# Kernel tuning notes

Hardware: AMD Instinct MI355X
Metric: run time of the kernel (lower is better)

The kernel has to match this reference:

```python
import jax, jax.numpy as jnp
import numpy as np

B, S, IN, H, OUT = 512, 1024, 32, 128, 1


def setup_inputs() -> dict:
    key = jax.random.key(0)
    ks = jax.random.split(key, 7)
    sc = 1.0 / np.sqrt(H)  # torch LSTM/Linear default init scale
    return {
        "x": jax.random.normal(ks[0], (B, S, IN), dtype=jnp.float32),
        "W_ih": jax.random.normal(ks[1], (4 * H, IN), dtype=jnp.float32) * sc,
        "W_hh": jax.random.normal(ks[2], (4 * H, H), dtype=jnp.float32) * sc,
        "b_ih": jax.random.normal(ks[3], (4 * H,), dtype=jnp.float32) * sc,
        "b_hh": jax.random.normal(ks[4], (4 * H,), dtype=jnp.float32) * sc,
        "W_lin": jax.random.normal(ks[5], (OUT, H * S), dtype=jnp.float32) * (1.0 / np.sqrt(H * S)),
        "b_lin": jax.random.normal(ks[6], (OUT,), dtype=jnp.float32) * (1.0 / np.sqrt(H * S)),
    }


def _lstm(x, W_ih, W_hh, b_ih, b_hh):
    # x: [B,S,IN]. Precompute input projection for all timesteps (one big GEMM).
    xw = jnp.einsum("bsi,gi->bsg", x, W_ih) + (b_ih + b_hh)  # [B,S,4H]
    h0 = jnp.zeros((x.shape[0], W_hh.shape[1]), dtype=x.dtype)
    c0 = jnp.zeros_like(h0)

    def step(carry, xw_t):
        h, c = carry
        gates = xw_t + h @ W_hh.T  # [B,4H]
        i, f, g, o = jnp.split(gates, 4, axis=-1)  # torch gate order i,f,g,o
        i = jax.nn.sigmoid(i)
        f = jax.nn.sigmoid(f)
        g = jnp.tanh(g)
        o = jax.nn.sigmoid(o)
        c = f * c + i * g
        h = o * jnp.tanh(c)
        return (h, c), h

    (_, _), hs = jax.lax.scan(step, (h0, c0), jnp.swapaxes(xw, 0, 1))  # hs: [S,B,H]
    return jnp.swapaxes(hs, 0, 1)  # [B,S,H]


def reference(x, W_ih, W_hh, b_ih, b_hh, W_lin, b_lin):
    lstm_out = _lstm(x, W_ih, W_hh, b_ih, b_hh)          # [B,S,H]
    flat = lstm_out.reshape(lstm_out.shape[0], -1)        # [B,S*H]
    return flat @ W_lin.T + b_lin                         # [B,OUT]
```

## Files before the change

### kernel.cpp

```cpp
#include <hip/hip_runtime.h>
#include <stdint.h>

constexpr int B = 512, S = 1024, IN = 32, H = 128;
constexpr int KTOT = IN + H;
constexpr int NJ = 4;
constexpr int KSL = KTOT / NJ;
constexpr int KP = KSL / 2;

typedef uint32_t u32;

__device__ __forceinline__ void dot2(float& c, u32 a, u32 b) {
  asm("v_dot2_f32_f16 %0, %1, %2, %0" : "+v"(c) : "v"(a), "v"(b));
}
__device__ __forceinline__ float sigm(float v) {
  float e = __builtin_amdgcn_exp2f(-1.4426950408889634f * v);
  return __builtin_amdgcn_rcpf(1.0f + e);
}
__device__ __forceinline__ float tanh_(float v) {
  float e = __builtin_amdgcn_exp2f(-2.8853900817779268f * v);
  return 2.0f * __builtin_amdgcn_rcpf(1.0f + e) - 1.0f;
}

__global__ __launch_bounds__(512, 4)
void lstm_fused(const float* __restrict__ x, const float* __restrict__ Wih,
                const float* __restrict__ Whh, const float* __restrict__ bih,
                const float* __restrict__ bhh, const float* __restrict__ Wlin,
                const float* __restrict__ blin, float* __restrict__ out) {
  __shared__ alignas(16) _Float16 hx[2][KTOT];
  __shared__ alignas(16) float red[NJ][H][4];
  __shared__ float redf[H];

  const int tid = threadIdx.x;
  const int lane = tid & 63;
  const int w = tid >> 6;
  const int j = w >> 1;
  const int g = (w & 1) * 64 + lane;
  const int b = blockIdx.x;
  const int par = b & 1;
  const int aw0 = par, aw1 = 6 + par;
  const bool isact = (w == aw0) || (w == aw1);
  const int ga = (w == aw0) ? lane : 64 + lane;
  const int xw = 2 + par;

  u32 wreg[4][KP];
#pragma unroll
  for (int c = 0; c < 4; ++c) {
    const int n = c * H + g;
#pragma unroll
    for (int pq = 0; pq < KP; ++pq) {
      const int k0 = KSL * j + 2 * pq, k1 = k0 + 1;
      const float f0 = (k0 < IN) ? Wih[n * IN + k0] : Whh[n * H + (k0 - IN)];
      const float f1 = (k1 < IN) ? Wih[n * IN + k1] : Whh[n * H + (k1 - IN)];
      union { _Float16 h[2]; u32 u; } cv;
      cv.h[0] = (_Float16)f0;
      cv.h[1] = (_Float16)f1;
      wreg[c][pq] = cv.u;
    }
  }
#pragma unroll
  for (int c = 0; c < 4; ++c)
#pragma unroll
    for (int pq = 0; pq < KP; ++pq) asm volatile("" : "+v"(wreg[c][pq]));

  float bias_a[4] = {0.f, 0.f, 0.f, 0.f};
  if (isact) {
#pragma unroll
    for (int c = 0; c < 4; ++c) bias_a[c] = bih[c * H + ga] + bhh[c * H + ga];
  }

  const size_t xbase = (size_t)b * S * IN;
  if (tid < KTOT) {
    hx[0][tid] = (tid < IN) ? (_Float16)x[xbase + tid] : (_Float16)0.0f;
    hx[1][tid] = (_Float16)0.0f;
  }
  __syncthreads();

  float cc = 0.f, oa = 0.f;

  for (int s = 0; s < S; ++s) {
    const int p = s & 1, np = p ^ 1;
    float wl = 0.f, xn = 0.f;
    if (isact) wl = Wlin[s * H + ga];
    const bool xload = (w == xw) && (lane < IN) && (s + 1 < S);
    if (xload) xn = x[xbase + (s + 1) * IN + lane];

    const uint4* pp =
        (const uint4*)((const char*)&hx[p][0] + j * (KSL * 2));
    float acc[4] = {0.f, 0.f, 0.f, 0.f};
#pragma unroll
    for (int q = 0; q < 5; ++q) {
      const uint4 v = pp[q];
      const u32 e[4] = {v.x, v.y, v.z, v.w};
#pragma unroll
      for (int u = 0; u < 4; ++u)
#pragma unroll
        for (int c = 0; c < 4; ++c) dot2(acc[c], e[u], wreg[c][4 * q + u]);
    }
    *(float4*)&red[j][g][0] = make_float4(acc[0], acc[1], acc[2], acc[3]);
    __syncthreads();

    if (isact) {
      const float4 r0 = *(const float4*)&red[0][ga][0];
      const float4 r1 = *(const float4*)&red[1][ga][0];
      const float4 r2 = *(const float4*)&red[2][ga][0];
      const float4 r3 = *(const float4*)&red[3][ga][0];
      const float gi = sigm(r0.x + r1.x + r2.x + r3.x + bias_a[0]);
      const float gf = sigm(r0.y + r1.y + r2.y + r3.y + bias_a[1]);
      const float gg = tanh_(r0.z + r1.z + r2.z + r3.z + bias_a[2]);
      const float go = sigm(r0.w + r1.w + r2.w + r3.w + bias_a[3]);
      cc = gf * cc + gi * gg;
      const float h = go * tanh_(cc);
      hx[np][IN + ga] = (_Float16)h;
      oa += h * wl;
    } else if (xload) {
      hx[np][lane] = (_Float16)xn;
    }
    __syncthreads();
  }

  if (isact) redf[ga] = oa;
  __syncthreads();
  if (tid == 0) {
    float sum = blin[0];
    for (int k = 0; k < H; ++k) sum += redf[k];
    out[b] = sum;
  }
}

extern "C" void kernel_launch(void* const* d_in, const int* in_sizes, int n_in,
                              void* d_out, int out_size, void* d_ws, size_t ws_size,
                              hipStream_t stream) {
  const float* x    = (const float*)d_in[0];
  const float* Wih  = (const float*)d_in[1];
  const float* Whh  = (const float*)d_in[2];
  const float* bih  = (const float*)d_in[3];
  const float* bhh  = (const float*)d_in[4];
  const float* Wlin = (const float*)d_in[5];
  const float* blin = (const float*)d_in[6];
  float* outp = (float*)d_out;
  hipLaunchKernelGGL(lstm_fused, dim3(B), dim3(512), 0, stream,
                     x, Wih, Whh, bih, bhh, Wlin, blin, outp);
}
```

Before: 1.264 ms.

## Process two batch rows per block with software-pipelined dot and activation phases

Each block now handles two sequences with 1024 threads. Each wave holds weights for only two gates, and the work is staggered so the activations of one row overlap the dot products of the other row inside each synchronisation interval. The aim is to hide the serial activation latency and the barrier stalls of the recurrence. In exchange, launch bounds drop to one block per CU, there are half as many blocks, and each wave does twice the dot work per step.

```diff
diff --git a/kernel.cpp b/kernel.cpp
--- a/kernel.cpp
+++ b/kernel.cpp
@@ -21,31 +21,34 @@
   return 2.0f * __builtin_amdgcn_rcpf(1.0f + e) - 1.0f;
 }
 
-__global__ __launch_bounds__(512, 4)
+__global__ __launch_bounds__(1024, 1)
 void lstm_fused(const float* __restrict__ x, const float* __restrict__ Wih,
                 const float* __restrict__ Whh, const float* __restrict__ bih,
                 const float* __restrict__ bhh, const float* __restrict__ Wlin,
                 const float* __restrict__ blin, float* __restrict__ out) {
-  __shared__ alignas(16) _Float16 hx[2][KTOT];
-  __shared__ alignas(16) float red[NJ][H][4];
-  __shared__ float redf[H];
+  __shared__ alignas(16) _Float16 hx0[2][KTOT];
+  __shared__ alignas(16) _Float16 hx1[2][KTOT];
+  __shared__ float red0[NJ][4][H];
+  __shared__ float red1[NJ][4][H];
+  __shared__ float redf[2][H];
 
   const int tid = threadIdx.x;
   const int lane = tid & 63;
   const int w = tid >> 6;
-  const int j = w >> 1;
+  const int j = w >> 2;
+  const int cp = (w >> 1) & 1;
   const int g = (w & 1) * 64 + lane;
-  const int b = blockIdx.x;
-  const int par = b & 1;
-  const int aw0 = par, aw1 = 6 + par;
-  const bool isact = (w == aw0) || (w == aw1);
-  const int ga = (w == aw0) ? lane : 64 + lane;
-  const int xw = 2 + par;
+  const int r0 = blockIdx.x * 2;
 
-  u32 wreg[4][KP];
+  const bool isact0 = (w == 0) || (w == 5);
+  const bool isact1 = (w == 10) || (w == 15);
+  const bool isact = isact0 || isact1;
+  const int ga = ((w == 5) || (w == 15)) ? 64 + lane : lane;
+
+  u32 wreg[2][KP];
 #pragma unroll
-  for (int c = 0; c < 4; ++c) {
-    const int n = c * H + g;
+  for (int c2 = 0; c2 < 2; ++c2) {
+    const int n = (2 * cp + c2) * H + g;
 #pragma unroll
     for (int pq = 0; pq < KP; ++pq) {
       const int k0 = KSL * j + 2 * pq, k1 = k0 + 1;
@@ -54,77 +57,103 @@
       union { _Float16 h[2]; u32 u; } cv;
       cv.h[0] = (_Float16)f0;
       cv.h[1] = (_Float16)f1;
-      wreg[c][pq] = cv.u;
+      wreg[c2][pq] = cv.u;
     }
   }
 #pragma unroll
-  for (int c = 0; c < 4; ++c)
+  for (int c2 = 0; c2 < 2; ++c2)
 #pragma unroll
-    for (int pq = 0; pq < KP; ++pq) asm volatile("" : "+v"(wreg[c][pq]));
+    for (int pq = 0; pq < KP; ++pq) asm volatile("" : "+v"(wreg[c2][pq]));
 
-  float bias_a[4] = {0.f, 0.f, 0.f, 0.f};
+  float bias[4] = {0.f, 0.f, 0.f, 0.f};
   if (isact) {
 #pragma unroll
-    for (int c = 0; c < 4; ++c) bias_a[c] = bih[c * H + ga] + bhh[c * H + ga];
+    for (int c = 0; c < 4; ++c) bias[c] = bih[c * H + ga] + bhh[c * H + ga];
   }
 
-  const size_t xbase = (size_t)b * S * IN;
+  const size_t xb0 = (size_t)r0 * S * IN, xb1 = (size_t)(r0 + 1) * S * IN;
   if (tid < KTOT) {
-    hx[0][tid] = (tid < IN) ? (_Float16)x[xbase + tid] : (_Float16)0.0f;
-    hx[1][tid] = (_Float16)0.0f;
+    hx0[0][tid] = (tid < IN) ? (_Float16)x[xb0 + tid] : (_Float16)0.0f;
+    hx0[1][tid] = (_Float16)0.0f;
+  } else if (tid < 2 * KTOT) {
+    const int t = tid - KTOT;
+    hx1[0][t] = (t < IN) ? (_Float16)x[xb1 + t] : (_Float16)0.0f;
+    hx1[1][t] = (_Float16)0.0f;
   }
   __syncthreads();
 
   float cc = 0.f, oa = 0.f;
 
+#define DOTS(HXBUF, REDBUF)                                             \
+  {                                                                     \
+    const uint4* pp = (const uint4*)((HXBUF) + j * KSL);                \
+    float a0 = 0.f, a1 = 0.f;                                           \
+    _Pragma("unroll") for (int q = 0; q < 5; ++q) {                     \
+      const uint4 v = pp[q];                                            \
+      dot2(a0, v.x, wreg[0][4 * q + 0]);                                \
+      dot2(a1, v.x, wreg[1][4 * q + 0]);                                \
+      dot2(a0, v.y, wreg[0][4 * q + 1]);                                \
+      dot2(a1, v.y, wreg[1][4 * q + 1]);                                \
+      dot2(a0, v.z, wreg[0][4 * q + 2]);                                \
+      dot2(a1, v.z, wreg[1][4 * q + 2]);                                \
+      dot2(a0, v.w, wreg[0][4 * q + 3]);                                \
+      dot2(a1, v.w, wreg[1][4 * q + 3]);                                \
+    }                                                                   \
+    (REDBUF)[j][2 * cp][g] = a0;                                        \
+    (REDBUF)[j][2 * cp + 1][g] = a1;                                    \
+  }
+
+#define ACT(REDBUF, HWRITE, WL)                                         \
+  {                                                                     \
+    const float s0 = (REDBUF)[0][0][ga] + (REDBUF)[1][0][ga] +          \
+                     (REDBUF)[2][0][ga] + (REDBUF)[3][0][ga] + bias[0]; \
+    const float s1 = (REDBUF)[0][1][ga] + (REDBUF)[1][1][ga] +          \
+                     (REDBUF)[2][1][ga] + (REDBUF)[3][1][ga] + bias[1]; \
+    const float s2 = (REDBUF)[0][2][ga] + (REDBUF)[1][2][ga] +          \
+                     (REDBUF)[2][2][ga] + (REDBUF)[3][2][ga] + bias[2]; \
+    const float s3 = (REDBUF)[0][3][ga] + (REDBUF)[1][3][ga] +          \
+                     (REDBUF)[2][3][ga] + (REDBUF)[3][3][ga] + bias[3]; \
+    const float gi = sigm(s0), gf = sigm(s1);                           \
+    const float gg = tanh_(s2), go = sigm(s3);                          \
+    cc = gf * cc + gi * gg;                                             \
+    const float h = go * tanh_(cc);                                     \
+    if (HWRITE) ((_Float16*)(HWRITE))[IN + ga] = (_Float16)h;           \
+    oa += h * (WL);                                                     \
+  }
+
   for (int s = 0; s < S; ++s) {
     const int p = s & 1, np = p ^ 1;
-    float wl = 0.f, xn = 0.f;
-    if (isact) wl = Wlin[s * H + ga];
-    const bool xload = (w == xw) && (lane < IN) && (s + 1 < S);
-    if (xload) xn = x[xbase + (s + 1) * IN + lane];
+    float wl = 0.f;
+    if (isact0) wl = Wlin[s * H + ga];
+    else if (isact1 && s > 0) wl = Wlin[(s - 1) * H + ga];
 
-    const uint4* pp =
-        (const uint4*)((const char*)&hx[p][0] + j * (KSL * 2));
-    float acc[4] = {0.f, 0.f, 0.f, 0.f};
-#pragma unroll
-    for (int q = 0; q < 5; ++q) {
-      const uint4 v = pp[q];
-      const u32 e[4] = {v.x, v.y, v.z, v.w};
-#pragma unroll
-      for (int u = 0; u < 4; ++u)
-#pragma unroll
-        for (int c = 0; c < 4; ++c) dot2(acc[c], e[u], wreg[c][4 * q + u]);
-    }
-    *(float4*)&red[j][g][0] = make_float4(acc[0], acc[1], acc[2], acc[3]);
+    DOTS(hx0[p], red0);
+    if (isact1 && s > 0) ACT(red1, hx1[p], wl);
     __syncthreads();
 
-    if (isact) {
-      const float4 r0 = *(const float4*)&red[0][ga][0];
-      const float4 r1 = *(const float4*)&red[1][ga][0];
-      const float4 r2 = *(const float4*)&red[2][ga][0];
-      const float4 r3 = *(const float4*)&red[3][ga][0];
-      const float gi = sigm(r0.x + r1.x + r2.x + r3.x + bias_a[0]);
-      const float gf = sigm(r0.y + r1.y + r2.y + r3.y + bias_a[1]);
-      const float gg = tanh_(r0.z + r1.z + r2.z + r3.z + bias_a[2]);
-      const float go = sigm(r0.w + r1.w + r2.w + r3.w + bias_a[3]);
-      cc = gf * cc + gi * gg;
-      const float h = go * tanh_(cc);
-      hx[np][IN + ga] = (_Float16)h;
-      oa += h * wl;
-    } else if (xload) {
-      hx[np][lane] = (_Float16)xn;
+    DOTS(hx1[p], red1);
+    if (isact0) ACT(red0, hx0[np], wl);
+    if ((w == 2) && (s + 1 < S)) {
+      const int row = lane >> 5, k = lane & 31;
+      const float xv = x[(row ? xb1 : xb0) + (size_t)(s + 1) * IN + k];
+      (row ? hx1 : hx0)[np][k] = (_Float16)xv;
     }
     __syncthreads();
   }
 
-  if (isact) redf[ga] = oa;
+  if (isact1) {
+    const float wlf = Wlin[(S - 1) * H + ga];
+    ACT(red1, (void*)0, wlf);
+  }
+  if (isact) redf[isact1 ? 1 : 0][ga] = oa;
   __syncthreads();
-  if (tid == 0) {
+  if (tid < 2) {
     float sum = blin[0];
-    for (int k = 0; k < H; ++k) sum += redf[k];
-    out[b] = sum;
+    for (int k = 0; k < H; ++k) sum += redf[tid][k];
+    out[r0 + tid] = sum;
   }
+#undef DOTS
+#undef ACT
 }
 
 extern "C" void kernel_launch(void* const* d_in, const int* in_sizes, int n_in,
@@ -138,6 +167,6 @@
   const float* Wlin = (const float*)d_in[5];
   const float* blin = (const float*)d_in[6];
   float* outp = (float*)d_out;
-  hipLaunchKernelGGL(lstm_fused, dim3(B), dim3(512), 0, stream,
+  hipLaunchKernelGGL(lstm_fused, dim3(B / 2), dim3(1024), 0, stream,
                      x, Wih, Whh, bih, bhh, Wlin, blin, outp);
 }
```

New measurement: 1.415 ms. +11.9%, slower.
